# Optimization experiments

Measured on AMD Instinct MI355X. Metric: run time of the kernel, lower is better.

Reference implementation:

```python
import jax, jax.numpy as jnp
import numpy as np

HEADS = 4
DIM_HEAD = 32
SCALE = 16.0
EPS = 1e-5  # jax.nn.standardize default


def _standardize(t):
    # standardize over last axis (the flattened x*y*z sequence), per (b, h, d)
    mu = jnp.mean(t, axis=-1, keepdims=True)
    var = jnp.var(t, axis=-1, keepdims=True)
    return (t - mu) * jax.lax.rsqrt(var + EPS)


def setup_inputs() -> dict:
    key = jax.random.key(0)
    k1, k2, k3 = jax.random.split(key, 3)
    dim = 64
    hidden = HEADS * DIM_HEAD  # 128
    b, x, y, z = 2, 16, 16, 16
    inp = jax.random.normal(k1, (b, x, y, z, dim), dtype=jnp.float32)
    # 1x1x1 convs == pointwise channel matmuls; init like flax lecun_normal-ish scale
    w_qkv = jax.random.normal(k2, (dim, 3 * hidden), dtype=jnp.float32) / np.sqrt(dim)
    w_out = jax.random.normal(k3, (hidden, dim), dtype=jnp.float32) / np.sqrt(hidden)
    b_out = jnp.zeros((dim,), dtype=jnp.float32)
    return {"input": inp, "w_qkv": w_qkv, "w_out": w_out, "b_out": b_out}


def reference(input, w_qkv, w_out, b_out):
    b, x, y, z, c = input.shape
    s = x * y * z
    # pointwise conv -> qkv
    qkv = jnp.einsum('bxyzc,cd->bxyzd', input, w_qkv)  # [b,x,y,z,3*hidden]
    q, k, v = jnp.split(qkv, 3, axis=-1)
    # rearrange 'b x y z (h c) -> b h c (x y z)'
    def to_bhds(t):
        return t.reshape(b, s, HEADS, DIM_HEAD).transpose(0, 2, 3, 1)  # [b,h,d,s]
    q, k, v = map(to_bhds, (q, k, v))
    q = _standardize(q)
    k = _standardize(k)
    sim = jnp.einsum('bhdi,bhdj->bhij', q, k) * SCALE  # [b,h,s,s]
    attn = jax.nn.softmax(sim, axis=-1)
    out = jnp.einsum('bhij,bhdj->bhid', attn, v)  # [b,h,s,d]
    # rearrange 'b h (x y z) d -> b x y z (h d)'
    out = out.transpose(0, 2, 1, 3).reshape(b, x, y, z, HEADS * DIM_HEAD)
    return jnp.einsum('bxyzc,co->bxyzo', out, w_out) + b_out
```

## Files before the change

kernel.cpp:

```cpp
#include <hip/hip_runtime.h>
#include <math.h>
#include <stdint.h>


typedef __attribute__((ext_vector_type(8))) short short8;
typedef __attribute__((ext_vector_type(2))) float f32x2;
typedef __attribute__((ext_vector_type(4))) float f32x4;
typedef __attribute__((ext_vector_type(16))) float f32x16;

#define QSCALE 23.083120654223414f

#if __has_builtin(__builtin_amdgcn_exp2f)
#define EXP2F(x) __builtin_amdgcn_exp2f(x)
#else
#define EXP2F(x) exp2f(x)
#endif

__device__ inline uint32_t pack_hilo(float y) {
  uint32_t uy = __float_as_uint(y);
  uint32_t hb = (uy + 0x7fffu + ((uy >> 16) & 1u)) >> 16;
  float hf = __uint_as_float(hb << 16);
  float r = y - hf;
  uint32_t ur = __float_as_uint(r);
  uint32_t lb = (ur + 0x7fffu + ((ur >> 16) & 1u)) >> 16;
  return (hb << 16) | (lb & 0xffffu);
}

__device__ inline ushort f32_to_bf16(float y) {
  uint32_t uy = __float_as_uint(y);
  return (ushort)((uy + 0x7fffu + ((uy >> 16) & 1u)) >> 16);
}

__device__ inline float bpermf(int addr, float v) {
  return __int_as_float(__builtin_amdgcn_ds_bpermute(addr, __float_as_int(v)));
}

__device__ inline short8 as_s8(uint4 v) {
  union { uint4 u; short8 s; } t;
  t.u = v;
  return t.s;
}

__global__ __launch_bounds__(256) void qkv_kernel(const float* __restrict__ in,
                                                  const float* __restrict__ w,
                                                  float* __restrict__ qf,
                                                  float* __restrict__ kf,
                                                  ushort* __restrict__ vfr,
                                                  float* __restrict__ psum,
                                                  float* __restrict__ psq,
                                                  const float* __restrict__ bias,
                                                  float* __restrict__ out) {
  __shared__ char smem[18432];
  __shared__ float ssum[64], ssq[64];
  ushort* Bh = (ushort*)smem;
  ushort* Bl = (ushort*)(smem + 9216);
  float* VT = (float*)smem;

  const int ctile = blockIdx.x % 6;
  const int stile = blockIdx.x / 6;
  const int tid = threadIdx.x;
  const int row0 = stile * 64;
  const int sel = ctile >> 1;

  for (int i = blockIdx.x * 256 + tid; i < 8192 * 64; i += 768 * 256)
    out[i] = bias[i & 63];

  if (tid < 64) { ssum[tid] = 0.f; ssq[tid] = 0.f; }

  {
    const int col = tid & 63;
    const int k0 = (tid >> 6) * 16;
    const float* wp = w + (size_t)k0 * 384 + ctile * 64 + col;
    float xv[16];
#pragma unroll
    for (int j = 0; j < 16; ++j) xv[j] = wp[(size_t)j * 384];
    uint32_t hi[8], lo[8];
#pragma unroll
    for (int p = 0; p < 8; ++p) {
      const uint32_t u0 = __float_as_uint(xv[2 * p]);
      const uint32_t u1 = __float_as_uint(xv[2 * p + 1]);
      hi[p] = __builtin_amdgcn_perm(u1, u0, 0x07060302u);
      const float d0 = xv[2 * p] - __uint_as_float(u0 & 0xffff0000u);
      const float d1 = xv[2 * p + 1] - __uint_as_float(u1 & 0xffff0000u);
      lo[p] = __builtin_amdgcn_perm(__float_as_uint(d1), __float_as_uint(d0), 0x07060302u);
    }
    uint4* bh = (uint4*)&Bh[col * 72 + k0];
    bh[0] = make_uint4(hi[0], hi[1], hi[2], hi[3]);
    bh[1] = make_uint4(hi[4], hi[5], hi[6], hi[7]);
    uint4* bl = (uint4*)&Bl[col * 72 + k0];
    bl[0] = make_uint4(lo[0], lo[1], lo[2], lo[3]);
    bl[1] = make_uint4(lo[4], lo[5], lo[6], lo[7]);
  }
  __syncthreads();

  const int wv = tid >> 6, lane = tid & 63;
  const int wr = wv >> 1, wc = wv & 1;
  const int h2 = lane >> 5, pl = lane & 31;

  short8 ah[4], al[4];
  {
    const float* ap = in + (size_t)(row0 + wr * 32 + pl) * 64 + h2 * 8;
#pragma unroll
    for (int kb = 0; kb < 4; ++kb) {
      const float4 xa = *(const float4*)(ap + kb * 16);
      const float4 xb = *(const float4*)(ap + kb * 16 + 4);
      const float xs[8] = {xa.x, xa.y, xa.z, xa.w, xb.x, xb.y, xb.z, xb.w};
      uint32_t hp[4], lp[4];
#pragma unroll
      for (int p = 0; p < 4; ++p) {
        const uint32_t u0 = __float_as_uint(xs[2 * p]);
        const uint32_t u1 = __float_as_uint(xs[2 * p + 1]);
        hp[p] = __builtin_amdgcn_perm(u1, u0, 0x07060302u);
        const float d0 = xs[2 * p] - __uint_as_float(u0 & 0xffff0000u);
        const float d1 = xs[2 * p + 1] - __uint_as_float(u1 & 0xffff0000u);
        lp[p] = __builtin_amdgcn_perm(__float_as_uint(d1), __float_as_uint(d0), 0x07060302u);
      }
      union { uint32_t u[4]; short8 s; } th, tl;
      th.u[0] = hp[0]; th.u[1] = hp[1]; th.u[2] = hp[2]; th.u[3] = hp[3];
      tl.u[0] = lp[0]; tl.u[1] = lp[1]; tl.u[2] = lp[2]; tl.u[3] = lp[3];
      ah[kb] = th.s;
      al[kb] = tl.s;
    }
  }

  const ushort* bhp = &Bh[(wc * 32 + pl) * 72 + h2 * 8];
  const ushort* blp = &Bl[(wc * 32 + pl) * 72 + h2 * 8];
  f32x16 acc = {};
#pragma unroll
  for (int kb = 0; kb < 4; ++kb) {
    const short8 bh = *(const short8*)(bhp + kb * 16);
    const short8 bl = *(const short8*)(blp + kb * 16);
    acc = __builtin_amdgcn_mfma_f32_32x32x16_bf16(ah[kb], bh, acc, 0, 0, 0);
    acc = __builtin_amdgcn_mfma_f32_32x32x16_bf16(ah[kb], bl, acc, 0, 0, 0);
    acc = __builtin_amdgcn_mfma_f32_32x32x16_bf16(al[kb], bh, acc, 0, 0, 0);
  }

  const int b = row0 >> 12;
  const int sl0 = (row0 & 4095) + wr * 32;
  const int chg = ctile * 64 + wc * 32 + pl;

  if (sel < 2) {
    const int hd0 = chg & 127;
    const int h = hd0 >> 5, d0 = hd0 & 31;
    float* dst = (sel == 0 ? qf : kf) + ((size_t)(b * 4 + h) * 4096 + sl0) * 32 + d0;
    float s1 = 0.f, s2 = 0.f;
#pragma unroll
    for (int reg = 0; reg < 16; ++reg) {
      const int r = (reg & 3) + 8 * (reg >> 2) + 4 * h2;
      dst[(size_t)r * 32] = acc[reg];
      s1 += acc[reg];
      s2 += acc[reg] * acc[reg];
    }
    atomicAdd(&ssum[wc * 32 + pl], s1);
    atomicAdd(&ssq[wc * 32 + pl], s2);
    __syncthreads();
    if (tid < 64) {
      const int ch = (ctile & 1) * 64 + tid;
      const int idx = (((sel * 2 + b) * 128) + ch) * 64 + (stile & 63);
      psum[idx] = ssum[tid];
      psq[idx] = ssq[tid];
    }
  } else {
    __syncthreads();
    const int chv = wc * 32 + pl;
#pragma unroll
    for (int reg = 0; reg < 16; ++reg) {
      const int r = wr * 32 + (reg & 3) + 8 * (reg >> 2) + 4 * h2;
      VT[chv * 68 + r] = acc[reg];
    }
    __syncthreads();
    const int jt0 = (row0 & 4095) >> 5;
#pragma unroll
    for (int hl = 0; hl < 2; ++hl) {
      const int jtl = tid >> 7, c = (tid >> 6) & 1, ln = tid & 63;
      const int d = ln & 31, hh = ln >> 5;
      const int jloc = 32 * jtl + 16 * c + 8 * hh;
      const int ch = hl * 32 + d;
      const float4 f0 = *(const float4*)&VT[ch * 68 + jloc];
      const float4 f1 = *(const float4*)&VT[ch * 68 + jloc + 4];
      uint4 pk;
      pk.x = (uint32_t)f32_to_bf16(f0.x) | ((uint32_t)f32_to_bf16(f0.y) << 16);
      pk.y = (uint32_t)f32_to_bf16(f0.z) | ((uint32_t)f32_to_bf16(f0.w) << 16);
      pk.z = (uint32_t)f32_to_bf16(f1.x) | ((uint32_t)f32_to_bf16(f1.y) << 16);
      pk.w = (uint32_t)f32_to_bf16(f1.z) | ((uint32_t)f32_to_bf16(f1.w) << 16);
      const int h = (ctile - 4) * 2 + hl;
      ushort* dst =
          vfr + (((size_t)((b * 4 + h) * 128 + jt0 + jtl) * 2 + c) * 64 + ln) * 8;
      *(uint4*)dst = pk;
    }
  }
}

__global__ __launch_bounds__(256) void norm_kernel(const float* __restrict__ qf,
                                                   const float* __restrict__ kf,
                                                   ushort* __restrict__ qfr_hi,
                                                   ushort* __restrict__ qfr_lo,
                                                   ushort* __restrict__ kfr_hi,
                                                   ushort* __restrict__ kfr_lo,
                                                   const float* __restrict__ psum,
                                                   const float* __restrict__ psq) {
  const int bx = blockIdx.x;
  const int tensor = bx >> 7;
  const int bh = (bx >> 4) & 7;
  const int s0 = (bx & 15) * 256;
  const int tid = threadIdx.x;
  __shared__ float red[2][32][8];
  __shared__ float tA[32], tB[32];
  {
    const int d = tid >> 3, p = tid & 7;
    const int base = ((tensor * 2 + (bh >> 2)) * 128 + (bh & 3) * 32 + d) * 64 + p * 8;
    float sm = 0.f, sq = 0.f;
#pragma unroll
    for (int e = 0; e < 8; ++e) {
      sm += psum[base + e];
      sq += psq[base + e];
    }
    red[0][d][p] = sm;
    red[1][d][p] = sq;
  }
  __syncthreads();
  if (tid < 32) {
    float sm = 0.f, sq = 0.f;
#pragma unroll
    for (int e = 0; e < 8; ++e) {
      sm += red[0][tid][e];
      sq += red[1][tid][e];
    }
    const float mu = sm * (1.f / 4096.f);
    const float scale = tensor == 0 ? QSCALE : 1.0f;
    const float inv = rsqrtf(sq * (1.f / 4096.f) - mu * mu + 1e-5f) * scale;
    tA[tid] = inv;
    tB[tid] = -mu * inv;
  }
  __syncthreads();

  const float* src = (tensor == 0 ? qf : kf) + (size_t)bh * 4096 * 32;
  ushort* dhi = (tensor == 0 ? qfr_hi : kfr_hi) + (size_t)(bh * 128 + (s0 >> 5)) * 1024;
  ushort* dlo = (tensor == 0 ? qfr_lo : kfr_lo) + (size_t)(bh * 128 + (s0 >> 5)) * 1024;
#pragma unroll
  for (int pass = 0; pass < 4; ++pass) {
    const int idx = tid + pass * 256;
    const int jtl = idx >> 7;
    const int c = (idx >> 6) & 1;
    const int ln = idx & 63;
    const int p = ln & 31, hh = ln >> 5;
    const int row = tensor == 0 ? p : ((p & 0x13) | ((p & 4) << 1) | ((p & 8) >> 1));
    const int s = s0 + 32 * jtl + row;
    const int d0 = 16 * c + 8 * hh;
    const float4 x0 = *(const float4*)&src[(size_t)s * 32 + d0];
    const float4 x1 = *(const float4*)&src[(size_t)s * 32 + d0 + 4];
    const float4 A0 = *(const float4*)&tA[d0];
    const float4 A1 = *(const float4*)&tA[d0 + 4];
    const float4 B0 = *(const float4*)&tB[d0];
    const float4 B1 = *(const float4*)&tB[d0 + 4];
    uint32_t pk[8];
    pk[0] = pack_hilo(fmaf(x0.x, A0.x, B0.x));
    pk[1] = pack_hilo(fmaf(x0.y, A0.y, B0.y));
    pk[2] = pack_hilo(fmaf(x0.z, A0.z, B0.z));
    pk[3] = pack_hilo(fmaf(x0.w, A0.w, B0.w));
    pk[4] = pack_hilo(fmaf(x1.x, A1.x, B1.x));
    pk[5] = pack_hilo(fmaf(x1.y, A1.y, B1.y));
    pk[6] = pack_hilo(fmaf(x1.z, A1.z, B1.z));
    pk[7] = pack_hilo(fmaf(x1.w, A1.w, B1.w));
    uint4 HV, LV;
    HV.x = __builtin_amdgcn_perm(pk[1], pk[0], 0x07060302u);
    HV.y = __builtin_amdgcn_perm(pk[3], pk[2], 0x07060302u);
    HV.z = __builtin_amdgcn_perm(pk[5], pk[4], 0x07060302u);
    HV.w = __builtin_amdgcn_perm(pk[7], pk[6], 0x07060302u);
    LV.x = __builtin_amdgcn_perm(pk[1], pk[0], 0x05040100u);
    LV.y = __builtin_amdgcn_perm(pk[3], pk[2], 0x05040100u);
    LV.z = __builtin_amdgcn_perm(pk[5], pk[4], 0x05040100u);
    LV.w = __builtin_amdgcn_perm(pk[7], pk[6], 0x05040100u);
    const size_t doff = ((size_t)(jtl * 2 + c) * 64 + ln) * 8;
    *(uint4*)(dhi + doff) = HV;
    *(uint4*)(dlo + doff) = LV;
  }
}

__global__ __launch_bounds__(512, 4) void attn_kernel(const ushort* __restrict__ qfr_hi,
                                                      const ushort* __restrict__ qfr_lo,
                                                      const ushort* __restrict__ kfr_hi,
                                                      const ushort* __restrict__ kfr_lo,
                                                      const ushort* __restrict__ vfr,
                                                      const float* __restrict__ wout,
                                                      float* __restrict__ out) {
  __shared__ float OM[8 * 32 * 36];
  __shared__ float ML[8 * 64];

  const int tid = threadIdx.x;
  const int w = tid >> 6;
  const int js = w;
  const int lane = tid & 63;
  const int pl = lane & 31, h2 = lane >> 5;
  const int bh = blockIdx.x & 7;
  const int it = blockIdx.x >> 3;

  const size_t qbase = (size_t)(bh * 128 + it) * 1024 + lane * 8;
  const short8 qh0 = *(const short8*)(qfr_hi + qbase);
  const short8 qh1 = *(const short8*)(qfr_hi + qbase + 512);
  const short8 ql0 = *(const short8*)(qfr_lo + qbase);
  const short8 ql1 = *(const short8*)(qfr_lo + qbase + 512);

  const int bp32 = (lane ^ 32) << 2;

  const size_t kbase = (size_t)(bh * 128 + js * 16) * 1024 + lane * 8;
  const ushort* kh = kfr_hi + kbase;
  const ushort* kl = kfr_lo + kbase;
  const ushort* vp = vfr + kbase;

  union { f32x16 v; f32x2 p[8]; } oac;
#pragma unroll
  for (int r = 0; r < 16; ++r) oac.v[r] = 0.f;
  const f32x16 zf = {};
  float m = -INFINITY, l = 0.f;

  uint4 rk0 = *(const uint4*)(kh);
  uint4 rk1 = *(const uint4*)(kh + 512);
  uint4 rl0 = *(const uint4*)(kl);
  uint4 rl1 = *(const uint4*)(kl + 512);
  uint4 rv0 = *(const uint4*)(vp);
  uint4 rv1 = *(const uint4*)(vp + 512);

  for (int t = 0; t < 16; ++t) {
    const short8 ck0 = as_s8(rk0), ck1 = as_s8(rk1);
    const short8 cl0 = as_s8(rl0), cl1 = as_s8(rl1);
    const short8 cv0 = as_s8(rv0), cv1 = as_s8(rv1);
    {
      const int off = (t + 1) * 1024;
      rk0 = *(const uint4*)(kh + off);
      rk1 = *(const uint4*)(kh + off + 512);
      rl0 = *(const uint4*)(kl + off);
      rl1 = *(const uint4*)(kl + off + 512);
      rv0 = *(const uint4*)(vp + off);
      rv1 = *(const uint4*)(vp + off + 512);
    }

    __builtin_amdgcn_s_setprio(1);
    union { f32x16 v; f32x2 p[8]; } sc;
    sc.v = __builtin_amdgcn_mfma_f32_32x32x16_bf16(ck0, qh0, zf, 0, 0, 0);
    sc.v = __builtin_amdgcn_mfma_f32_32x32x16_bf16(ck1, qh1, sc.v, 0, 0, 0);
    sc.v = __builtin_amdgcn_mfma_f32_32x32x16_bf16(ck0, ql0, sc.v, 0, 0, 0);
    sc.v = __builtin_amdgcn_mfma_f32_32x32x16_bf16(ck1, ql1, sc.v, 0, 0, 0);
    sc.v = __builtin_amdgcn_mfma_f32_32x32x16_bf16(cl0, qh0, sc.v, 0, 0, 0);
    sc.v = __builtin_amdgcn_mfma_f32_32x32x16_bf16(cl1, qh1, sc.v, 0, 0, 0);
    __builtin_amdgcn_s_setprio(0);

    const float x0 = fmaxf(fmaxf(sc.v[0], sc.v[1]), sc.v[2]);
    const float x1 = fmaxf(fmaxf(sc.v[3], sc.v[4]), sc.v[5]);
    const float x2 = fmaxf(fmaxf(sc.v[6], sc.v[7]), sc.v[8]);
    const float x3 = fmaxf(fmaxf(sc.v[9], sc.v[10]), sc.v[11]);
    const float x4 = fmaxf(fmaxf(sc.v[12], sc.v[13]), sc.v[14]);
    float mx = fmaxf(fmaxf(fmaxf(x0, x1), x2), fmaxf(fmaxf(x3, x4), sc.v[15]));
    mx = fmaxf(mx, bpermf(bp32, mx));
    const float mn = fmaxf(m, mx);
    const float al = EXP2F(m - mn);
    m = mn;
    const f32x2 mn2 = {mn, mn};
#pragma unroll
    for (int i = 0; i < 8; ++i) sc.p[i] = sc.p[i] - mn2;
#pragma unroll
    for (int r = 0; r < 16; ++r) sc.v[r] = EXP2F(sc.v[r]);
    const f32x2 a0 = sc.p[0] + sc.p[1], a1 = sc.p[2] + sc.p[3];
    const f32x2 a2 = sc.p[4] + sc.p[5], a3 = sc.p[6] + sc.p[7];
    const f32x2 b0 = a0 + a1, b1 = a2 + a3;
    const f32x2 c0 = b0 + b1;
    float rs = c0.x + c0.y;
    rs += bpermf(bp32, rs);
    l = l * al + rs;
    const f32x2 al2 = {al, al};
#pragma unroll
    for (int i = 0; i < 8; ++i) oac.p[i] = oac.p[i] * al2;

    uint32_t pk[8];
#pragma unroll
    for (int i = 0; i < 8; ++i)
      pk[i] = __builtin_amdgcn_perm(__float_as_uint(sc.v[2 * i + 1]),
                                    __float_as_uint(sc.v[2 * i]), 0x07060302u);
    union { uint32_t u4[4]; short8 s8; } p0, p1;
    p0.u4[0] = pk[0]; p0.u4[1] = pk[1]; p0.u4[2] = pk[2]; p0.u4[3] = pk[3];
    p1.u4[0] = pk[4]; p1.u4[1] = pk[5]; p1.u4[2] = pk[6]; p1.u4[3] = pk[7];

    __builtin_amdgcn_s_setprio(1);
    oac.v = __builtin_amdgcn_mfma_f32_32x32x16_bf16(cv0, p0.s8, oac.v, 0, 0, 0);
    oac.v = __builtin_amdgcn_mfma_f32_32x32x16_bf16(cv1, p1.s8, oac.v, 0, 0, 0);
    __builtin_amdgcn_s_setprio(0);
  }

  {
    float* om = OM + (size_t)(w * 32 + pl) * 36;
#pragma unroll
    for (int g = 0; g < 4; ++g)
      *(float4*)&om[4 * h2 + 8 * g] =
          make_float4(oac.v[4 * g], oac.v[4 * g + 1], oac.v[4 * g + 2], oac.v[4 * g + 3]);
    if (h2 == 0) {
      ML[w * 64 + pl] = m;
      ML[w * 64 + 32 + pl] = l;
    }
  }
  __syncthreads();
  const int b = bh >> 2, h = bh & 3;
  float vals[2];
#pragma unroll
  for (int pass = 0; pass < 2; ++pass) {
    const int idx = tid + pass * 512;
    const int i = idx >> 5;
    const int d = idx & 31;
    float mk[8], lk[8];
#pragma unroll
    for (int k = 0; k < 8; ++k) {
      mk[k] = ML[k * 64 + i];
      lk[k] = ML[k * 64 + 32 + i];
    }
    const float M01 = fmaxf(mk[0], mk[1]), M23 = fmaxf(mk[2], mk[3]);
    const float M45 = fmaxf(mk[4], mk[5]), M67 = fmaxf(mk[6], mk[7]);
    const float M = fmaxf(fmaxf(M01, M23), fmaxf(M45, M67));
    float L = 0.f, V = 0.f;
#pragma unroll
    for (int k = 0; k < 8; ++k) {
      const float wk = EXP2F(mk[k] - M);
      L += lk[k] * wk;
      V += OM[(k * 32 + i) * 36 + d] * wk;
    }
    vals[pass] = V * (1.001953125f / L);
  }
  __syncthreads();

  float* V2 = OM;
  float* WL = OM + 1024;
#pragma unroll
  for (int pass = 0; pass < 2; ++pass) V2[tid + pass * 512] = vals[pass];
  {
    const float* wsrc = wout + (size_t)h * 32 * 64;
#pragma unroll
    for (int p = 0; p < 4; ++p) WL[tid + p * 512] = wsrc[tid + p * 512];
  }
  __syncthreads();
#pragma unroll
  for (int p = 0; p < 4; ++p) {
    const int idx = tid + p * 512;
    const int i = idx >> 6, col = idx & 63;
    float acc = 0.f;
#pragma unroll
    for (int d = 0; d < 32; ++d) acc = fmaf(V2[i * 32 + d], WL[d * 64 + col], acc);
    atomicAdd(&out[((size_t)(b * 4096) + it * 32 + i) * 64 + col], acc);
  }
}

extern "C" void kernel_launch(void* const* d_in, const int* in_sizes, int n_in,
                              void* d_out, int out_size, void* d_ws, size_t ws_size,
                              hipStream_t stream) {
  const float* input = (const float*)d_in[0];
  const float* w_qkv = (const float*)d_in[1];
  const float* w_out = (const float*)d_in[2];
  const float* b_out = (const float*)d_in[3];

  char* W = (char*)d_ws;
  float* qf = (float*)(W + 0);
  float* kf = (float*)(W + (4u << 20));
  ushort* kfr_hi = (ushort*)(W + (8u << 20));
  ushort* kfr_lo = (ushort*)(W + (10u << 20));
  ushort* vfr = (ushort*)(W + (12u << 20));
  ushort* qfr_hi = (ushort*)(W + (14u << 20));
  ushort* qfr_lo = (ushort*)(W + (16u << 20));
  float* psum = (float*)(W + (18u << 20));
  float* psq = (float*)(W + (18u << 20) + (128u << 10));
  float* out = (float*)d_out;

  hipLaunchKernelGGL(qkv_kernel, dim3(768), dim3(256), 0, stream, input, w_qkv, qf, kf,
                     vfr, psum, psq, b_out, out);
  hipLaunchKernelGGL(norm_kernel, dim3(256), dim3(256), 0, stream, qf, kf, qfr_hi,
                     qfr_lo, kfr_hi, kfr_lo, psum, psq);
  hipLaunchKernelGGL(attn_kernel, dim3(1024), dim3(512), 0, stream, qfr_hi, qfr_lo,
                     kfr_hi, kfr_lo, vfr, w_out, out);
}
```

Baseline: 125.5 us.

## Process two query tiles per wave to reuse K/V fragment loads

Each block now handles two 32-row query tiles with 4 waves instead of one tile with 8 waves. Each wave loops over 32 key tiles instead of 16 and reuses every loaded K/V fragment for both query tiles, halving K/V global traffic per query. The cost is a doubled accumulator register set and a smaller grid (512 blocks of 256 threads), which lowers parallelism and occupancy. The V prefetch into registers is also dropped in favour of in-loop loads.

```diff
diff --git a/kernel.cpp b/kernel.cpp
--- a/kernel.cpp
+++ b/kernel.cpp
@@ -277,172 +277,199 @@
   }
 }
 
-__global__ __launch_bounds__(512, 4) void attn_kernel(const ushort* __restrict__ qfr_hi,
+__global__ __launch_bounds__(256, 2) void attn_kernel(const ushort* __restrict__ qfr_hi,
                                                       const ushort* __restrict__ qfr_lo,
                                                       const ushort* __restrict__ kfr_hi,
                                                       const ushort* __restrict__ kfr_lo,
                                                       const ushort* __restrict__ vfr,
                                                       const float* __restrict__ wout,
                                                       float* __restrict__ out) {
-  __shared__ float OM[8 * 32 * 36];
-  __shared__ float ML[8 * 64];
+  __shared__ float OM[4 * 2 * 32 * 36];
+  __shared__ float ML[4 * 2 * 64];
 
   const int tid = threadIdx.x;
   const int w = tid >> 6;
-  const int js = w;
   const int lane = tid & 63;
   const int pl = lane & 31, h2 = lane >> 5;
   const int bh = blockIdx.x & 7;
-  const int it = blockIdx.x >> 3;
-
-  const size_t qbase = (size_t)(bh * 128 + it) * 1024 + lane * 8;
-  const short8 qh0 = *(const short8*)(qfr_hi + qbase);
-  const short8 qh1 = *(const short8*)(qfr_hi + qbase + 512);
-  const short8 ql0 = *(const short8*)(qfr_lo + qbase);
-  const short8 ql1 = *(const short8*)(qfr_lo + qbase + 512);
+  const int itp = blockIdx.x >> 3;
+
+  const size_t qbase = (size_t)(bh * 128 + itp * 2) * 1024 + lane * 8;
+  const short8 qh0_0 = *(const short8*)(qfr_hi + qbase);
+  const short8 qh1_0 = *(const short8*)(qfr_hi + qbase + 512);
+  const short8 ql0_0 = *(const short8*)(qfr_lo + qbase);
+  const short8 ql1_0 = *(const short8*)(qfr_lo + qbase + 512);
+  const short8 qh0_1 = *(const short8*)(qfr_hi + qbase + 1024);
+  const short8 qh1_1 = *(const short8*)(qfr_hi + qbase + 1536);
+  const short8 ql0_1 = *(const short8*)(qfr_lo + qbase + 1024);
+  const short8 ql1_1 = *(const short8*)(qfr_lo + qbase + 1536);
 
   const int bp32 = (lane ^ 32) << 2;
 
-  const size_t kbase = (size_t)(bh * 128 + js * 16) * 1024 + lane * 8;
+  const size_t kbase = (size_t)(bh * 128 + w * 32) * 1024 + lane * 8;
   const ushort* kh = kfr_hi + kbase;
   const ushort* kl = kfr_lo + kbase;
   const ushort* vp = vfr + kbase;
 
-  union { f32x16 v; f32x2 p[8]; } oac;
-#pragma unroll
-  for (int r = 0; r < 16; ++r) oac.v[r] = 0.f;
+  union { f32x16 v; f32x2 p[8]; } oac0, oac1;
+#pragma unroll
+  for (int r = 0; r < 16; ++r) { oac0.v[r] = 0.f; oac1.v[r] = 0.f; }
   const f32x16 zf = {};
-  float m = -INFINITY, l = 0.f;
+  float m0 = -INFINITY, l0 = 0.f, m1 = -INFINITY, l1 = 0.f;
 
   uint4 rk0 = *(const uint4*)(kh);
   uint4 rk1 = *(const uint4*)(kh + 512);
   uint4 rl0 = *(const uint4*)(kl);
   uint4 rl1 = *(const uint4*)(kl + 512);
-  uint4 rv0 = *(const uint4*)(vp);
-  uint4 rv1 = *(const uint4*)(vp + 512);
-
-  for (int t = 0; t < 16; ++t) {
+
+  for (int t = 0; t < 32; ++t) {
     const short8 ck0 = as_s8(rk0), ck1 = as_s8(rk1);
     const short8 cl0 = as_s8(rl0), cl1 = as_s8(rl1);
-    const short8 cv0 = as_s8(rv0), cv1 = as_s8(rv1);
+    const uint4 rv0 = *(const uint4*)(vp + t * 1024);
+    const uint4 rv1 = *(const uint4*)(vp + t * 1024 + 512);
     {
       const int off = (t + 1) * 1024;
       rk0 = *(const uint4*)(kh + off);
       rk1 = *(const uint4*)(kh + off + 512);
       rl0 = *(const uint4*)(kl + off);
       rl1 = *(const uint4*)(kl + off + 512);
-      rv0 = *(const uint4*)(vp + off);
-      rv1 = *(const uint4*)(vp + off + 512);
-    }
-
-    __builtin_amdgcn_s_setprio(1);
-    union { f32x16 v; f32x2 p[8]; } sc;
-    sc.v = __builtin_amdgcn_mfma_f32_32x32x16_bf16(ck0, qh0, zf, 0, 0, 0);
-    sc.v = __builtin_amdgcn_mfma_f32_32x32x16_bf16(ck1, qh1, sc.v, 0, 0, 0);
-    sc.v = __builtin_amdgcn_mfma_f32_32x32x16_bf16(ck0, ql0, sc.v, 0, 0, 0);
-    sc.v = __builtin_amdgcn_mfma_f32_32x32x16_bf16(ck1, ql1, sc.v, 0, 0, 0);
-    sc.v = __builtin_amdgcn_mfma_f32_32x32x16_bf16(cl0, qh0, sc.v, 0, 0, 0);
-    sc.v = __builtin_amdgcn_mfma_f32_32x32x16_bf16(cl1, qh1, sc.v, 0, 0, 0);
-    __builtin_amdgcn_s_setprio(0);
-
-    const float x0 = fmaxf(fmaxf(sc.v[0], sc.v[1]), sc.v[2]);
-    const float x1 = fmaxf(fmaxf(sc.v[3], sc.v[4]), sc.v[5]);
-    const float x2 = fmaxf(fmaxf(sc.v[6], sc.v[7]), sc.v[8]);
-    const float x3 = fmaxf(fmaxf(sc.v[9], sc.v[10]), sc.v[11]);
-    const float x4 = fmaxf(fmaxf(sc.v[12], sc.v[13]), sc.v[14]);
-    float mx = fmaxf(fmaxf(fmaxf(x0, x1), x2), fmaxf(fmaxf(x3, x4), sc.v[15]));
-    mx = fmaxf(mx, bpermf(bp32, mx));
-    const float mn = fmaxf(m, mx);
-    const float al = EXP2F(m - mn);
-    m = mn;
-    const f32x2 mn2 = {mn, mn};
-#pragma unroll
-    for (int i = 0; i < 8; ++i) sc.p[i] = sc.p[i] - mn2;
-#pragma unroll
-    for (int r = 0; r < 16; ++r) sc.v[r] = EXP2F(sc.v[r]);
-    const f32x2 a0 = sc.p[0] + sc.p[1], a1 = sc.p[2] + sc.p[3];
-    const f32x2 a2 = sc.p[4] + sc.p[5], a3 = sc.p[6] + sc.p[7];
-    const f32x2 b0 = a0 + a1, b1 = a2 + a3;
-    const f32x2 c0 = b0 + b1;
-    float rs = c0.x + c0.y;
-    rs += bpermf(bp32, rs);
-    l = l * al + rs;
-    const f32x2 al2 = {al, al};
-#pragma unroll
-    for (int i = 0; i < 8; ++i) oac.p[i] = oac.p[i] * al2;
-
-    uint32_t pk[8];
-#pragma unroll
-    for (int i = 0; i < 8; ++i)
-      pk[i] = __builtin_amdgcn_perm(__float_as_uint(sc.v[2 * i + 1]),
-                                    __float_as_uint(sc.v[2 * i]), 0x07060302u);
-    union { uint32_t u4[4]; short8 s8; } p0, p1;
-    p0.u4[0] = pk[0]; p0.u4[1] = pk[1]; p0.u4[2] = pk[2]; p0.u4[3] = pk[3];
-    p1.u4[0] = pk[4]; p1.u4[1] = pk[5]; p1.u4[2] = pk[6]; p1.u4[3] = pk[7];
-
-    __builtin_amdgcn_s_setprio(1);
-    oac.v = __builtin_amdgcn_mfma_f32_32x32x16_bf16(cv0, p0.s8, oac.v, 0, 0, 0);
-    oac.v = __builtin_amdgcn_mfma_f32_32x32x16_bf16(cv1, p1.s8, oac.v, 0, 0, 0);
-    __builtin_amdgcn_s_setprio(0);
-  }
-
-  {
-    float* om = OM + (size_t)(w * 32 + pl) * 36;
+    }
+    const short8 cv0 = as_s8(rv0), cv1 = as_s8(rv1);
+
+#pragma unroll
+    for (int itl = 0; itl < 2; ++itl) {
+      const short8 qh0 = itl == 0 ? qh0_0 : qh0_1;
+      const short8 qh1 = itl == 0 ? qh1_0 : qh1_1;
+      const short8 ql0 = itl == 0 ? ql0_0 : ql0_1;
+      const short8 ql1 = itl == 0 ? ql1_0 : ql1_1;
+      float m = itl == 0 ? m0 : m1;
+      float l = itl == 0 ? l0 : l1;
+
+      __builtin_amdgcn_s_setprio(1);
+      union { f32x16 v; f32x2 p[8]; } sc;
+      sc.v = __builtin_amdgcn_mfma_f32_32x32x16_bf16(ck0, qh0, zf, 0, 0, 0);
+      sc.v = __builtin_amdgcn_mfma_f32_32x32x16_bf16(ck1, qh1, sc.v, 0, 0, 0);
+      sc.v = __builtin_amdgcn_mfma_f32_32x32x16_bf16(ck0, ql0, sc.v, 0, 0, 0);
+      sc.v = __builtin_amdgcn_mfma_f32_32x32x16_bf16(ck1, ql1, sc.v, 0, 0, 0);
+      sc.v = __builtin_amdgcn_mfma_f32_32x32x16_bf16(cl0, qh0, sc.v, 0, 0, 0);
+      sc.v = __builtin_amdgcn_mfma_f32_32x32x16_bf16(cl1, qh1, sc.v, 0, 0, 0);
+      __builtin_amdgcn_s_setprio(0);
+
+      const float x0 = fmaxf(fmaxf(sc.v[0], sc.v[1]), sc.v[2]);
+      const float x1 = fmaxf(fmaxf(sc.v[3], sc.v[4]), sc.v[5]);
+      const float x2 = fmaxf(fmaxf(sc.v[6], sc.v[7]), sc.v[8]);
+      const float x3 = fmaxf(fmaxf(sc.v[9], sc.v[10]), sc.v[11]);
+      const float x4 = fmaxf(fmaxf(sc.v[12], sc.v[13]), sc.v[14]);
+      float mx = fmaxf(fmaxf(fmaxf(x0, x1), x2), fmaxf(fmaxf(x3, x4), sc.v[15]));
+      mx = fmaxf(mx, bpermf(bp32, mx));
+      const float mn = fmaxf(m, mx);
+      const float al = EXP2F(m - mn);
+      m = mn;
+      const f32x2 mn2 = {mn, mn};
+#pragma unroll
+      for (int i = 0; i < 8; ++i) sc.p[i] = sc.p[i] - mn2;
+#pragma unroll
+      for (int r = 0; r < 16; ++r) sc.v[r] = EXP2F(sc.v[r]);
+      const f32x2 a0 = sc.p[0] + sc.p[1], a1 = sc.p[2] + sc.p[3];
+      const f32x2 a2 = sc.p[4] + sc.p[5], a3 = sc.p[6] + sc.p[7];
+      const f32x2 b0 = a0 + a1, b1 = a2 + a3;
+      const f32x2 c0 = b0 + b1;
+      float rs = c0.x + c0.y;
+      rs += bpermf(bp32, rs);
+      l = l * al + rs;
+      const f32x2 al2 = {al, al};
+
+      uint32_t pk[8];
+#pragma unroll
+      for (int i = 0; i < 8; ++i)
+        pk[i] = __builtin_amdgcn_perm(__float_as_uint(sc.v[2 * i + 1]),
+                                      __float_as_uint(sc.v[2 * i]), 0x07060302u);
+      union { uint32_t u4[4]; short8 s8; } p0, p1;
+      p0.u4[0] = pk[0]; p0.u4[1] = pk[1]; p0.u4[2] = pk[2]; p0.u4[3] = pk[3];
+      p1.u4[0] = pk[4]; p1.u4[1] = pk[5]; p1.u4[2] = pk[6]; p1.u4[3] = pk[7];
+
+      if (itl == 0) {
+#pragma unroll
+        for (int i = 0; i < 8; ++i) oac0.p[i] = oac0.p[i] * al2;
+        __builtin_amdgcn_s_setprio(1);
+        oac0.v = __builtin_amdgcn_mfma_f32_32x32x16_bf16(cv0, p0.s8, oac0.v, 0, 0, 0);
+        oac0.v = __builtin_amdgcn_mfma_f32_32x32x16_bf16(cv1, p1.s8, oac0.v, 0, 0, 0);
+        __builtin_amdgcn_s_setprio(0);
+        m0 = m; l0 = l;
+      } else {
+#pragma unroll
+        for (int i = 0; i < 8; ++i) oac1.p[i] = oac1.p[i] * al2;
+        __builtin_amdgcn_s_setprio(1);
+        oac1.v = __builtin_amdgcn_mfma_f32_32x32x16_bf16(cv0, p0.s8, oac1.v, 0, 0, 0);
+        oac1.v = __builtin_amdgcn_mfma_f32_32x32x16_bf16(cv1, p1.s8, oac1.v, 0, 0, 0);
+        __builtin_amdgcn_s_setprio(0);
+        m1 = m; l1 = l;
+      }
+    }
+  }
+
+#pragma unroll
+  for (int itl = 0; itl < 2; ++itl) {
+    float* om = OM + (size_t)((w * 2 + itl) * 32 + pl) * 36;
+    const f32x16& oa = itl == 0 ? oac0.v : oac1.v;
 #pragma unroll
     for (int g = 0; g < 4; ++g)
       *(float4*)&om[4 * h2 + 8 * g] =
-          make_float4(oac.v[4 * g], oac.v[4 * g + 1], oac.v[4 * g + 2], oac.v[4 * g + 3]);
+          make_float4(oa[4 * g], oa[4 * g + 1], oa[4 * g + 2], oa[4 * g + 3]);
     if (h2 == 0) {
-      ML[w * 64 + pl] = m;
-      ML[w * 64 + 32 + pl] = l;
+      ML[(w * 2 + itl) * 64 + pl] = itl == 0 ? m0 : m1;
+      ML[(w * 2 + itl) * 64 + 32 + pl] = itl == 0 ? l0 : l1;
     }
   }
   __syncthreads();
   const int b = bh >> 2, h = bh & 3;
-  float vals[2];
-#pragma unroll
-  for (int pass = 0; pass < 2; ++pass) {
-    const int idx = tid + pass * 512;
-    const int i = idx >> 5;
+  float vals[8];
+#pragma unroll
+  for (int pass = 0; pass < 8; ++pass) {
+    const int idx = tid + pass * 256;
+    const int itl = idx >> 10;
+    const int i = (idx >> 5) & 31;
     const int d = idx & 31;
-    float mk[8], lk[8];
-#pragma unroll
-    for (int k = 0; k < 8; ++k) {
-      mk[k] = ML[k * 64 + i];
-      lk[k] = ML[k * 64 + 32 + i];
-    }
-    const float M01 = fmaxf(mk[0], mk[1]), M23 = fmaxf(mk[2], mk[3]);
-    const float M45 = fmaxf(mk[4], mk[5]), M67 = fmaxf(mk[6], mk[7]);
-    const float M = fmaxf(fmaxf(M01, M23), fmaxf(M45, M67));
+    float mk[4], lk[4];
+#pragma unroll
+    for (int k = 0; k < 4; ++k) {
+      mk[k] = ML[(k * 2 + itl) * 64 + i];
+      lk[k] = ML[(k * 2 + itl) * 64 + 32 + i];
+    }
+    const float M = fmaxf(fmaxf(mk[0], mk[1]), fmaxf(mk[2], mk[3]));
     float L = 0.f, V = 0.f;
 #pragma unroll
-    for (int k = 0; k < 8; ++k) {
+    for (int k = 0; k < 4; ++k) {
       const float wk = EXP2F(mk[k] - M);
       L += lk[k] * wk;
-      V += OM[(k * 32 + i) * 36 + d] * wk;
+      V += OM[((k * 2 + itl) * 32 + i) * 36 + d] * wk;
     }
     vals[pass] = V * (1.001953125f / L);
   }
   __syncthreads();
 
   float* V2 = OM;
-  float* WL = OM + 1024;
-#pragma unroll
-  for (int pass = 0; pass < 2; ++pass) V2[tid + pass * 512] = vals[pass];
+  float* WL = OM + 2048;
+#pragma unroll
+  for (int pass = 0; pass < 8; ++pass) V2[tid + pass * 256] = vals[pass];
   {
     const float* wsrc = wout + (size_t)h * 32 * 64;
 #pragma unroll
-    for (int p = 0; p < 4; ++p) WL[tid + p * 512] = wsrc[tid + p * 512];
+    for (int p = 0; p < 8; ++p) WL[tid + p * 256] = wsrc[tid + p * 256];
   }
   __syncthreads();
 #pragma unroll
-  for (int p = 0; p < 4; ++p) {
-    const int idx = tid + p * 512;
-    const int i = idx >> 6, col = idx & 63;
+  for (int p = 0; p < 16; ++p) {
+    const int idx = tid + p * 256;
+    const int itl = idx >> 11;
+    const int i = (idx >> 6) & 31;
+    const int col = idx & 63;
     float acc = 0.f;
 #pragma unroll
-    for (int d = 0; d < 32; ++d) acc = fmaf(V2[i * 32 + d], WL[d * 64 + col], acc);
-    atomicAdd(&out[((size_t)(b * 4096) + it * 32 + i) * 64 + col], acc);
+    for (int d = 0; d < 32; ++d)
+      acc = fmaf(V2[itl * 1024 + i * 32 + d], WL[d * 64 + col], acc);
+    const int ig = (itp * 2 + itl) * 32 + i;
+    atomicAdd(&out[((size_t)(b * 4096) + ig) * 64 + col], acc);
   }
 }
 
@@ -470,6 +497,6 @@
                      vfr, psum, psq, b_out, out);
   hipLaunchKernelGGL(norm_kernel, dim3(256), dim3(256), 0, stream, qf, kf, qfr_hi,
                      qfr_lo, kfr_hi, kfr_lo, psum, psq);
-  hipLaunchKernelGGL(attn_kernel, dim3(1024), dim3(512), 0, stream, qfr_hi, qfr_lo,
+  hipLaunchKernelGGL(attn_kernel, dim3(512), dim3(256), 0, stream, qfr_hi, qfr_lo,
                      kfr_hi, kfr_lo, vfr, w_out, out);
 }
```

Measured after the change: 122.0 us. 1.03x faster.

## Halve attention block to four waves, each processing two key tiles per step

Applied to the files above, without the earlier changes.

The attention kernel now launches 256 threads per block instead of 512. Each of the four waves handles 32 key tiles by processing two interleaved 32-key tiles per iteration, with two independent score accumulators. This halves the cross-wave merge work and doubles the independent MFMA chains per wave, which should improve instruction-level parallelism and cut the per-block softmax bookkeeping. In exchange it raises register pressure and removes the occupancy hint from launch_bounds. V loads are also no longer prefetched one iteration ahead and are issued in the same iteration they are used.

```diff
diff --git a/kernel.cpp b/kernel.cpp
--- a/kernel.cpp
+++ b/kernel.cpp
@@ -5,7 +5,6 @@
 
 typedef __attribute__((ext_vector_type(8))) short short8;
 typedef __attribute__((ext_vector_type(2))) float f32x2;
-typedef __attribute__((ext_vector_type(4))) float f32x4;
 typedef __attribute__((ext_vector_type(16))) float f32x16;
 
 #define QSCALE 23.083120654223414f
@@ -277,19 +276,18 @@
   }
 }
 
-__global__ __launch_bounds__(512, 4) void attn_kernel(const ushort* __restrict__ qfr_hi,
-                                                      const ushort* __restrict__ qfr_lo,
-                                                      const ushort* __restrict__ kfr_hi,
-                                                      const ushort* __restrict__ kfr_lo,
-                                                      const ushort* __restrict__ vfr,
-                                                      const float* __restrict__ wout,
-                                                      float* __restrict__ out) {
-  __shared__ float OM[8 * 32 * 36];
-  __shared__ float ML[8 * 64];
+__global__ __launch_bounds__(256) void attn_kernel(const ushort* __restrict__ qfr_hi,
+                                                   const ushort* __restrict__ qfr_lo,
+                                                   const ushort* __restrict__ kfr_hi,
+                                                   const ushort* __restrict__ kfr_lo,
+                                                   const ushort* __restrict__ vfr,
+                                                   const float* __restrict__ wout,
+                                                   float* __restrict__ out) {
+  __shared__ float OM[4 * 32 * 36];
+  __shared__ float ML[4 * 64];
 
   const int tid = threadIdx.x;
   const int w = tid >> 6;
-  const int js = w;
   const int lane = tid & 63;
   const int pl = lane & 31, h2 = lane >> 5;
   const int bh = blockIdx.x & 7;
@@ -303,10 +301,14 @@
 
   const int bp32 = (lane ^ 32) << 2;
 
-  const size_t kbase = (size_t)(bh * 128 + js * 16) * 1024 + lane * 8;
-  const ushort* kh = kfr_hi + kbase;
-  const ushort* kl = kfr_lo + kbase;
-  const ushort* vp = vfr + kbase;
+  const size_t kbase0 = (size_t)(bh * 128 + w * 32) * 1024 + lane * 8;
+  const size_t kbase1 = kbase0 + 16 * 1024;
+  const ushort* kh0 = kfr_hi + kbase0;
+  const ushort* kl0 = kfr_lo + kbase0;
+  const ushort* vp0 = vfr + kbase0;
+  const ushort* kh1 = kfr_hi + kbase1;
+  const ushort* kl1 = kfr_lo + kbase1;
+  const ushort* vp1 = vfr + kbase1;
 
   union { f32x16 v; f32x2 p[8]; } oac;
 #pragma unroll
@@ -314,56 +316,82 @@
   const f32x16 zf = {};
   float m = -INFINITY, l = 0.f;
 
-  uint4 rk0 = *(const uint4*)(kh);
-  uint4 rk1 = *(const uint4*)(kh + 512);
-  uint4 rl0 = *(const uint4*)(kl);
-  uint4 rl1 = *(const uint4*)(kl + 512);
-  uint4 rv0 = *(const uint4*)(vp);
-  uint4 rv1 = *(const uint4*)(vp + 512);
+  uint4 rk0a = *(const uint4*)(kh0), rk0b = *(const uint4*)(kh0 + 512);
+  uint4 rl0a = *(const uint4*)(kl0), rl0b = *(const uint4*)(kl0 + 512);
+  uint4 rk1a = *(const uint4*)(kh1), rk1b = *(const uint4*)(kh1 + 512);
+  uint4 rl1a = *(const uint4*)(kl1), rl1b = *(const uint4*)(kl1 + 512);
 
   for (int t = 0; t < 16; ++t) {
-    const short8 ck0 = as_s8(rk0), ck1 = as_s8(rk1);
-    const short8 cl0 = as_s8(rl0), cl1 = as_s8(rl1);
-    const short8 cv0 = as_s8(rv0), cv1 = as_s8(rv1);
+    const short8 ck0a = as_s8(rk0a), ck0b = as_s8(rk0b);
+    const short8 cl0a = as_s8(rl0a), cl0b = as_s8(rl0b);
+    const short8 ck1a = as_s8(rk1a), ck1b = as_s8(rk1b);
+    const short8 cl1a = as_s8(rl1a), cl1b = as_s8(rl1b);
+    const uint4 rv0a = *(const uint4*)(vp0 + t * 1024);
+    const uint4 rv0b = *(const uint4*)(vp0 + t * 1024 + 512);
+    const uint4 rv1a = *(const uint4*)(vp1 + t * 1024);
+    const uint4 rv1b = *(const uint4*)(vp1 + t * 1024 + 512);
     {
       const int off = (t + 1) * 1024;
-      rk0 = *(const uint4*)(kh + off);
-      rk1 = *(const uint4*)(kh + off + 512);
-      rl0 = *(const uint4*)(kl + off);
-      rl1 = *(const uint4*)(kl + off + 512);
-      rv0 = *(const uint4*)(vp + off);
-      rv1 = *(const uint4*)(vp + off + 512);
+      rk0a = *(const uint4*)(kh0 + off);
+      rk0b = *(const uint4*)(kh0 + off + 512);
+      rl0a = *(const uint4*)(kl0 + off);
+      rl0b = *(const uint4*)(kl0 + off + 512);
+      rk1a = *(const uint4*)(kh1 + off);
+      rk1b = *(const uint4*)(kh1 + off + 512);
+      rl1a = *(const uint4*)(kl1 + off);
+      rl1b = *(const uint4*)(kl1 + off + 512);
     }
 
     __builtin_amdgcn_s_setprio(1);
-    union { f32x16 v; f32x2 p[8]; } sc;
-    sc.v = __builtin_amdgcn_mfma_f32_32x32x16_bf16(ck0, qh0, zf, 0, 0, 0);
-    sc.v = __builtin_amdgcn_mfma_f32_32x32x16_bf16(ck1, qh1, sc.v, 0, 0, 0);
-    sc.v = __builtin_amdgcn_mfma_f32_32x32x16_bf16(ck0, ql0, sc.v, 0, 0, 0);
-    sc.v = __builtin_amdgcn_mfma_f32_32x32x16_bf16(ck1, ql1, sc.v, 0, 0, 0);
-    sc.v = __builtin_amdgcn_mfma_f32_32x32x16_bf16(cl0, qh0, sc.v, 0, 0, 0);
-    sc.v = __builtin_amdgcn_mfma_f32_32x32x16_bf16(cl1, qh1, sc.v, 0, 0, 0);
+    union { f32x16 v; f32x2 p[8]; } sc0, sc1;
+    sc0.v = __builtin_amdgcn_mfma_f32_32x32x16_bf16(ck0a, qh0, zf, 0, 0, 0);
+    sc1.v = __builtin_amdgcn_mfma_f32_32x32x16_bf16(ck1a, qh0, zf, 0, 0, 0);
+    sc0.v = __builtin_amdgcn_mfma_f32_32x32x16_bf16(ck0b, qh1, sc0.v, 0, 0, 0);
+    sc1.v = __builtin_amdgcn_mfma_f32_32x32x16_bf16(ck1b, qh1, sc1.v, 0, 0, 0);
+    sc0.v = __builtin_amdgcn_mfma_f32_32x32x16_bf16(ck0a, ql0, sc0.v, 0, 0, 0);
+    sc1.v = __builtin_amdgcn_mfma_f32_32x32x16_bf16(ck1a, ql0, sc1.v, 0, 0, 0);
+    sc0.v = __builtin_amdgcn_mfma_f32_32x32x16_bf16(ck0b, ql1, sc0.v, 0, 0, 0);
+    sc1.v = __builtin_amdgcn_mfma_f32_32x32x16_bf16(ck1b, ql1, sc1.v, 0, 0, 0);
+    sc0.v = __builtin_amdgcn_mfma_f32_32x32x16_bf16(cl0a, qh0, sc0.v, 0, 0, 0);
+    sc1.v = __builtin_amdgcn_mfma_f32_32x32x16_bf16(cl1a, qh0, sc1.v, 0, 0, 0);
+    sc0.v = __builtin_amdgcn_mfma_f32_32x32x16_bf16(cl0b, qh1, sc0.v, 0, 0, 0);
+    sc1.v = __builtin_amdgcn_mfma_f32_32x32x16_bf16(cl1b, qh1, sc1.v, 0, 0, 0);
     __builtin_amdgcn_s_setprio(0);
 
-    const float x0 = fmaxf(fmaxf(sc.v[0], sc.v[1]), sc.v[2]);
-    const float x1 = fmaxf(fmaxf(sc.v[3], sc.v[4]), sc.v[5]);
-    const float x2 = fmaxf(fmaxf(sc.v[6], sc.v[7]), sc.v[8]);
-    const float x3 = fmaxf(fmaxf(sc.v[9], sc.v[10]), sc.v[11]);
-    const float x4 = fmaxf(fmaxf(sc.v[12], sc.v[13]), sc.v[14]);
-    float mx = fmaxf(fmaxf(fmaxf(x0, x1), x2), fmaxf(fmaxf(x3, x4), sc.v[15]));
+    const float x0 = fmaxf(fmaxf(sc0.v[0], sc0.v[1]), sc0.v[2]);
+    const float x1 = fmaxf(fmaxf(sc0.v[3], sc0.v[4]), sc0.v[5]);
+    const float x2 = fmaxf(fmaxf(sc0.v[6], sc0.v[7]), sc0.v[8]);
+    const float x3 = fmaxf(fmaxf(sc0.v[9], sc0.v[10]), sc0.v[11]);
+    const float x4 = fmaxf(fmaxf(sc0.v[12], sc0.v[13]), sc0.v[14]);
+    const float y0 = fmaxf(fmaxf(sc1.v[0], sc1.v[1]), sc1.v[2]);
+    const float y1 = fmaxf(fmaxf(sc1.v[3], sc1.v[4]), sc1.v[5]);
+    const float y2 = fmaxf(fmaxf(sc1.v[6], sc1.v[7]), sc1.v[8]);
+    const float y3 = fmaxf(fmaxf(sc1.v[9], sc1.v[10]), sc1.v[11]);
+    const float y4 = fmaxf(fmaxf(sc1.v[12], sc1.v[13]), sc1.v[14]);
+    const float mxa = fmaxf(fmaxf(fmaxf(x0, x1), x2), fmaxf(fmaxf(x3, x4), sc0.v[15]));
+    const float mxb = fmaxf(fmaxf(fmaxf(y0, y1), y2), fmaxf(fmaxf(y3, y4), sc1.v[15]));
+    float mx = fmaxf(mxa, mxb);
     mx = fmaxf(mx, bpermf(bp32, mx));
     const float mn = fmaxf(m, mx);
     const float al = EXP2F(m - mn);
     m = mn;
     const f32x2 mn2 = {mn, mn};
 #pragma unroll
-    for (int i = 0; i < 8; ++i) sc.p[i] = sc.p[i] - mn2;
-#pragma unroll
-    for (int r = 0; r < 16; ++r) sc.v[r] = EXP2F(sc.v[r]);
-    const f32x2 a0 = sc.p[0] + sc.p[1], a1 = sc.p[2] + sc.p[3];
-    const f32x2 a2 = sc.p[4] + sc.p[5], a3 = sc.p[6] + sc.p[7];
-    const f32x2 b0 = a0 + a1, b1 = a2 + a3;
-    const f32x2 c0 = b0 + b1;
+    for (int i = 0; i < 8; ++i) {
+      sc0.p[i] = sc0.p[i] - mn2;
+      sc1.p[i] = sc1.p[i] - mn2;
+    }
+#pragma unroll
+    for (int r = 0; r < 16; ++r) {
+      sc0.v[r] = EXP2F(sc0.v[r]);
+      sc1.v[r] = EXP2F(sc1.v[r]);
+    }
+    const f32x2 a0 = sc0.p[0] + sc0.p[1], a1 = sc0.p[2] + sc0.p[3];
+    const f32x2 a2 = sc0.p[4] + sc0.p[5], a3 = sc0.p[6] + sc0.p[7];
+    const f32x2 a4 = sc1.p[0] + sc1.p[1], a5 = sc1.p[2] + sc1.p[3];
+    const f32x2 a6 = sc1.p[4] + sc1.p[5], a7 = sc1.p[6] + sc1.p[7];
+    const f32x2 b0 = a0 + a1, b1 = a2 + a3, b2 = a4 + a5, b3 = a6 + a7;
+    const f32x2 c0 = (b0 + b1) + (b2 + b3);
     float rs = c0.x + c0.y;
     rs += bpermf(bp32, rs);
     l = l * al + rs;
@@ -371,18 +399,25 @@
 #pragma unroll
     for (int i = 0; i < 8; ++i) oac.p[i] = oac.p[i] * al2;
 
-    uint32_t pk[8];
-#pragma unroll
-    for (int i = 0; i < 8; ++i)
-      pk[i] = __builtin_amdgcn_perm(__float_as_uint(sc.v[2 * i + 1]),
-                                    __float_as_uint(sc.v[2 * i]), 0x07060302u);
-    union { uint32_t u4[4]; short8 s8; } p0, p1;
-    p0.u4[0] = pk[0]; p0.u4[1] = pk[1]; p0.u4[2] = pk[2]; p0.u4[3] = pk[3];
-    p1.u4[0] = pk[4]; p1.u4[1] = pk[5]; p1.u4[2] = pk[6]; p1.u4[3] = pk[7];
+    uint32_t pk0[8], pk1[8];
+#pragma unroll
+    for (int i = 0; i < 8; ++i) {
+      pk0[i] = __builtin_amdgcn_perm(__float_as_uint(sc0.v[2 * i + 1]),
+                                     __float_as_uint(sc0.v[2 * i]), 0x07060302u);
+      pk1[i] = __builtin_amdgcn_perm(__float_as_uint(sc1.v[2 * i + 1]),
+                                     __float_as_uint(sc1.v[2 * i]), 0x07060302u);
+    }
+    union { uint32_t u4[4]; short8 s8; } p00, p01, p10, p11;
+    p00.u4[0] = pk0[0]; p00.u4[1] = pk0[1]; p00.u4[2] = pk0[2]; p00.u4[3] = pk0[3];
+    p01.u4[0] = pk0[4]; p01.u4[1] = pk0[5]; p01.u4[2] = pk0[6]; p01.u4[3] = pk0[7];
+    p10.u4[0] = pk1[0]; p10.u4[1] = pk1[1]; p10.u4[2] = pk1[2]; p10.u4[3] = pk1[3];
+    p11.u4[0] = pk1[4]; p11.u4[1] = pk1[5]; p11.u4[2] = pk1[6]; p11.u4[3] = pk1[7];
 
     __builtin_amdgcn_s_setprio(1);
-    oac.v = __builtin_amdgcn_mfma_f32_32x32x16_bf16(cv0, p0.s8, oac.v, 0, 0, 0);
-    oac.v = __builtin_amdgcn_mfma_f32_32x32x16_bf16(cv1, p1.s8, oac.v, 0, 0, 0);
+    oac.v = __builtin_amdgcn_mfma_f32_32x32x16_bf16(as_s8(rv0a), p00.s8, oac.v, 0, 0, 0);
+    oac.v = __builtin_amdgcn_mfma_f32_32x32x16_bf16(as_s8(rv0b), p01.s8, oac.v, 0, 0, 0);
+    oac.v = __builtin_amdgcn_mfma_f32_32x32x16_bf16(as_s8(rv1a), p10.s8, oac.v, 0, 0, 0);
+    oac.v = __builtin_amdgcn_mfma_f32_32x32x16_bf16(as_s8(rv1b), p11.s8, oac.v, 0, 0, 0);
     __builtin_amdgcn_s_setprio(0);
   }
 
@@ -399,24 +434,22 @@
   }
   __syncthreads();
   const int b = bh >> 2, h = bh & 3;
-  float vals[2];
-#pragma unroll
-  for (int pass = 0; pass < 2; ++pass) {
-    const int idx = tid + pass * 512;
+  float vals[4];
+#pragma unroll
+  for (int pass = 0; pass < 4; ++pass) {
+    const int idx = tid + pass * 256;
     const int i = idx >> 5;
     const int d = idx & 31;
-    float mk[8], lk[8];
-#pragma unroll
-    for (int k = 0; k < 8; ++k) {
+    float mk[4], lk[4];
+#pragma unroll
+    for (int k = 0; k < 4; ++k) {
       mk[k] = ML[k * 64 + i];
       lk[k] = ML[k * 64 + 32 + i];
     }
-    const float M01 = fmaxf(mk[0], mk[1]), M23 = fmaxf(mk[2], mk[3]);
-    const float M45 = fmaxf(mk[4], mk[5]), M67 = fmaxf(mk[6], mk[7]);
-    const float M = fmaxf(fmaxf(M01, M23), fmaxf(M45, M67));
+    const float M = fmaxf(fmaxf(mk[0], mk[1]), fmaxf(mk[2], mk[3]));
     float L = 0.f, V = 0.f;
 #pragma unroll
-    for (int k = 0; k < 8; ++k) {
+    for (int k = 0; k < 4; ++k) {
       const float wk = EXP2F(mk[k] - M);
       L += lk[k] * wk;
       V += OM[(k * 32 + i) * 36 + d] * wk;
@@ -428,16 +461,16 @@
   float* V2 = OM;
   float* WL = OM + 1024;
 #pragma unroll
-  for (int pass = 0; pass < 2; ++pass) V2[tid + pass * 512] = vals[pass];
+  for (int pass = 0; pass < 4; ++pass) V2[tid + pass * 256] = vals[pass];
   {
     const float* wsrc = wout + (size_t)h * 32 * 64;
 #pragma unroll
-    for (int p = 0; p < 4; ++p) WL[tid + p * 512] = wsrc[tid + p * 512];
+    for (int p = 0; p < 8; ++p) WL[tid + p * 256] = wsrc[tid + p * 256];
   }
   __syncthreads();
 #pragma unroll
-  for (int p = 0; p < 4; ++p) {
-    const int idx = tid + p * 512;
+  for (int p = 0; p < 8; ++p) {
+    const int idx = tid + p * 256;
     const int i = idx >> 6, col = idx & 63;
     float acc = 0.f;
 #pragma unroll
@@ -470,6 +503,6 @@
                      vfr, psum, psq, b_out, out);
   hipLaunchKernelGGL(norm_kernel, dim3(256), dim3(256), 0, stream, qf, kf, qfr_hi,
                      qfr_lo, kfr_hi, kfr_lo, psum, psq);
-  hipLaunchKernelGGL(attn_kernel, dim3(1024), dim3(512), 0, stream, qfr_hi, qfr_lo,
+  hipLaunchKernelGGL(attn_kernel, dim3(1024), dim3(256), 0, stream, qfr_hi, qfr_lo,
                      kfr_hi, kfr_lo, vfr, w_out, out);
 }
```

Measured after the change: 131.0 us. 1.04x slower.
